# Kernel tuning notes

Measured on AMD Instinct MI355X. Metric: run time of the kernel, lower is better.

## Reference

```python
import jax, jax.numpy as jnp
import numpy as np

N, D, H, DK, DEG = 8192, 512, 8, 64, 16
E = N * DEG
M = N


def setup_inputs() -> dict:
    key = jax.random.key(0)
    ks = jax.random.split(key, 12)
    x = jax.random.normal(ks[0], (N, D), dtype=jnp.float32)
    # every node has DEG neighbors -> sorted row index, random cols
    row_index = jnp.repeat(jnp.arange(N, dtype=jnp.int64), DEG)
    col_index = jax.random.randint(ks[1], (E,), 0, M, dtype=jnp.int64)
    to_col_index = jax.random.randint(ks[2], (M,), 0, N, dtype=jnp.int64)
    att_bias = 0.1 * jax.random.normal(ks[3], (H, E), dtype=jnp.float32)
    pos = 10.0 * jax.random.uniform(ks[4], (N, 3), dtype=jnp.float32)
    col_pos = 10.0 * jax.random.uniform(ks[5], (M, 3), dtype=jnp.float32)
    dist = jnp.linalg.norm(col_pos[col_index] - pos[row_index], axis=-1)
    s = 1.0 / np.sqrt(D)
    Wq = s * jax.random.normal(ks[6], (H, DK, D), dtype=jnp.float32)
    Wqv = s * jax.random.normal(ks[7], (H, 3, D), dtype=jnp.float32)
    Wk = s * jax.random.normal(ks[8], (H, DK, D), dtype=jnp.float32)
    Wv = s * jax.random.normal(ks[9], (H, DK, D), dtype=jnp.float32)
    Wout = s * jax.random.normal(ks[10], (D, D + 4 * H), dtype=jnp.float32)
    bout = jnp.zeros((D,), dtype=jnp.float32)
    return {"x": x, "row_index": row_index, "col_index": col_index,
            "to_col_index": to_col_index, "att_bias": att_bias, "dist": dist,
            "pos": pos, "col_pos": col_pos, "Wq": Wq, "Wqv": Wqv, "Wk": Wk,
            "Wv": Wv, "Wout": Wout, "bout": bout}


def reference(x, row_index, col_index, to_col_index, att_bias, dist, pos,
              col_pos, Wq, Wqv, Wk, Wv, Wout, bout):
    n = x.shape[0]
    dk = Wq.shape[1]
    scale = 1.0 / jnp.sqrt(jnp.asarray(dk, x.dtype))
    # per-head projections: [H, N, dk]
    q = jnp.einsum('nd,hkd->hnk', x, Wq) * scale
    qv = jnp.einsum('nd,hkd->hnk', x, Wqv)              # [H, N, 3]
    kx = jnp.einsum('nd,hkd->hnk', x, Wk)[:, to_col_index]  # [H, M, dk]
    vx = jnp.einsum('nd,hkd->hnk', x, Wv)[:, to_col_index]
    # gather per edge -> [E, H, *]
    qe = q[:, row_index].transpose(1, 0, 2)
    ke = kx[:, col_index].transpose(1, 0, 2)
    qve = qv[:, row_index].transpose(1, 0, 2)           # [E, H, 3]
    rel = col_pos[col_index] - pos[row_index]           # [E, 3]
    dist_e = jnp.where(dist == 0, jnp.inf, dist)        # masked_fill(dist==0, inf)
    # angular = qv_row . col_pos_col - qv_row . pos_row = qv_row . rel
    angular = jnp.einsum('ehc,ec->eh', qve, rel)
    logit = jnp.einsum('ehk,ehk->eh', qe, ke) + att_bias.T + angular / dist_e[:, None]
    # sparse (per-row segment) softmax
    m = jax.ops.segment_max(logit, row_index, num_segments=n)
    p = jnp.exp(logit - m[row_index])
    s = jax.ops.segment_sum(p, row_index, num_segments=n)
    att = p / s[row_index]                              # [E, H]
    natt = att / dist_e[:, None]
    dst_vec = jax.ops.segment_sum(natt[:, :, None] * col_pos[col_index][:, None, :],
                                  row_index, num_segments=n)   # [N, H, 3]
    avg_inv_dist = jax.ops.segment_sum(natt, row_index, num_segments=n)  # [N, H]
    src_vec = avg_inv_dist[:, :, None] * pos[:, None, :]
    diff = dst_vec - src_vec
    feat3 = diff / jnp.maximum(jnp.linalg.norm(diff, axis=-1, keepdims=True), 1e-12)
    ve = vx[:, col_index].transpose(1, 0, 2)            # [E, H, dk]
    y = jax.ops.segment_sum(att[:, :, None] * ve, row_index, num_segments=n)  # [N, H, dk]
    feat = jnp.concatenate([y, feat3, avg_inv_dist[:, :, None]], axis=-1)
    feat = feat.reshape(n, -1)                          # [N, H*(dk+4)]
    return feat @ Wout.T + bout
```

## Files before the change

kernel.cpp:

```cpp
#include <hip/hip_runtime.h>
#include <math.h>

#define N_NODES 8192
#define D_FEAT  512
#define DEG     16
#define E_EDGES (N_NODES * DEG)
#define FEAT_W  576
#define FEAT_USED 544
#define OUT_W   512
#define QKV_W   1664

typedef unsigned short u16;
typedef __attribute__((ext_vector_type(8))) short short8;
typedef __attribute__((ext_vector_type(8))) unsigned short us8;
typedef __attribute__((ext_vector_type(4))) float f32x4;

__device__ __forceinline__ u16 f2bf(float f) {
    union { float f; unsigned u; } c; c.f = f;
    unsigned u = c.u;
    unsigned r = u + 0x7FFFu + ((u >> 16) & 1u);
    return (u16)(r >> 16);
}
__device__ __forceinline__ float bf2f(u16 h) {
    union { unsigned u; float f; } c; c.u = ((unsigned)h) << 16;
    return c.f;
}

__device__ __forceinline__ void async16(const void* g, void* l) {
    __builtin_amdgcn_global_load_lds(
        (const __attribute__((address_space(1))) void*)g,
        (__attribute__((address_space(3))) void*)l, 16, 0, 0);
}

__global__ __launch_bounds__(256) void gemm_qkv(
    const u16* __restrict__ xh, const u16* __restrict__ Bfuse,
    u16* __restrict__ qkv)
{
    __shared__ u16 smem[128 * 64 * 2];
    u16* sA = smem;
    u16* sB = smem + 128 * 64;

    const int tid = threadIdx.x;
    const int flat = blockIdx.x;
    const int xcd = flat & 7;
    const int rr  = flat >> 3;
    const int bm  = (xcd + 8 * (rr / 13)) * 128;
    const int bn  = (rr % 13) * 128;

    const int wave = tid >> 6;
    const int lane = tid & 63;
    const int wr   = (wave >> 1) * 64;
    const int wc   = (wave & 1) * 64;
    const int lrow = lane & 15;
    const int quad = lane >> 4;

    f32x4 acc[4][4];
    #pragma unroll
    for (int i = 0; i < 4; ++i)
        #pragma unroll
        for (int j = 0; j < 4; ++j) {
            f32x4 z = {0.f, 0.f, 0.f, 0.f};
            acc[i][j] = z;
        }

    for (int k0 = 0; k0 < 512; k0 += 64) {
        #pragma unroll
        for (int i = 0; i < 4; ++i) {
            const int lin = i * 256 + tid;
            const int row = lin >> 3;
            const int seg = ((lin & 7) ^ (row & 7)) << 3;
            async16(xh    + (size_t)(bm + row) * 512 + k0 + seg, sA + (lin << 3));
            async16(Bfuse + (size_t)(bn + row) * 512 + k0 + seg, sB + (lin << 3));
        }
        __syncthreads();

        #pragma unroll
        for (int ko = 0; ko < 64; ko += 32) {
            const int cbase = ko >> 3;
            short8 a_h[4], b_h[4];
            #pragma unroll
            for (int t = 0; t < 4; ++t) {
                const int ra = wr + t * 16 + lrow;
                const int rb = wc + t * 16 + lrow;
                a_h[t] = *(const short8*)&sA[ra * 64 + (((cbase + quad) ^ (ra & 7)) << 3)];
                b_h[t] = *(const short8*)&sB[rb * 64 + (((cbase + quad) ^ (rb & 7)) << 3)];
            }
            #pragma unroll
            for (int mt = 0; mt < 4; ++mt)
                #pragma unroll
                for (int nt = 0; nt < 4; ++nt)
                    acc[mt][nt] = __builtin_amdgcn_mfma_f32_16x16x32_bf16(
                        a_h[mt], b_h[nt], acc[mt][nt], 0, 0, 0);
        }
        __syncthreads();
    }

    u16* sC = smem;
    #pragma unroll
    for (int nt = 0; nt < 4; ++nt) {
        const int col = wc + nt * 16 + lrow;
        #pragma unroll
        for (int mt = 0; mt < 4; ++mt)
            #pragma unroll
            for (int r = 0; r < 4; ++r) {
                const int row = wr + mt * 16 + quad * 4 + r;
                sC[row * 128 + col] = f2bf(acc[mt][nt][r]);
            }
    }
    __syncthreads();
    #pragma unroll
    for (int p = 0; p < 8; ++p) {
        const int lin = p * 256 + tid;
        const int row = lin >> 4;
        const int c16 = lin & 15;
        *(uint4*)(qkv + (size_t)(bm + row) * QKV_W + bn + c16 * 8) =
            *(const uint4*)&sC[row * 128 + c16 * 8];
    }
}

__global__ __launch_bounds__(256) void gemm_out(
    const u16* __restrict__ feat, const u16* __restrict__ Woth,
    const float* __restrict__ bout, float* __restrict__ out)
{
    __shared__ u16 smem[64 * 64 + 128 * 64];
    u16* sA = smem;
    u16* sB = smem + 64 * 64;

    const int tid = threadIdx.x;
    const int flat = blockIdx.x;
    const int xcd = flat & 7;
    const int rr  = flat >> 3;
    const int bm  = (xcd + 8 * (rr / 4)) * 64;
    const int bn  = (rr % 4) * 128;

    const int wave = tid >> 6;
    const int lane = tid & 63;
    const int wr   = (wave >> 1) * 32;
    const int wc   = (wave & 1) * 64;
    const int lrow = lane & 15;
    const int quad = lane >> 4;

    f32x4 acc[2][4];
    #pragma unroll
    for (int i = 0; i < 2; ++i)
        #pragma unroll
        for (int j = 0; j < 4; ++j) {
            f32x4 z = {0.f, 0.f, 0.f, 0.f};
            acc[i][j] = z;
        }

    for (int k0 = 0; k0 < FEAT_W; k0 += 64) {
        #pragma unroll
        for (int i = 0; i < 2; ++i) {
            const int lin = i * 256 + tid;
            const int row = lin >> 3;
            const int seg = ((lin & 7) ^ (row & 7)) << 3;
            async16(feat + (size_t)(bm + row) * FEAT_W + k0 + seg, sA + (lin << 3));
        }
        #pragma unroll
        for (int i = 0; i < 4; ++i) {
            const int lin = i * 256 + tid;
            const int row = lin >> 3;
            const int seg = ((lin & 7) ^ (row & 7)) << 3;
            async16(Woth + (size_t)(bn + row) * FEAT_W + k0 + seg, sB + (lin << 3));
        }
        __syncthreads();

        #pragma unroll
        for (int ko = 0; ko < 64; ko += 32) {
            const int cbase = ko >> 3;
            short8 a_h[2], b_h[4];
            #pragma unroll
            for (int t = 0; t < 2; ++t) {
                const int ra = wr + t * 16 + lrow;
                a_h[t] = *(const short8*)&sA[ra * 64 + (((cbase + quad) ^ (ra & 7)) << 3)];
            }
            #pragma unroll
            for (int t = 0; t < 4; ++t) {
                const int rb = wc + t * 16 + lrow;
                b_h[t] = *(const short8*)&sB[rb * 64 + (((cbase + quad) ^ (rb & 7)) << 3)];
            }
            #pragma unroll
            for (int mt = 0; mt < 2; ++mt)
                #pragma unroll
                for (int nt = 0; nt < 4; ++nt)
                    acc[mt][nt] = __builtin_amdgcn_mfma_f32_16x16x32_bf16(
                        a_h[mt], b_h[nt], acc[mt][nt], 0, 0, 0);
        }
        __syncthreads();
    }

    #pragma unroll
    for (int nt = 0; nt < 4; ++nt) {
        const int col = bn + wc + nt * 16 + lrow;
        const float bb = bout[col];
        #pragma unroll
        for (int mt = 0; mt < 2; ++mt)
            #pragma unroll
            for (int r = 0; r < 4; ++r) {
                const int row = bm + wr + mt * 16 + quad * 4 + r;
                out[(size_t)row * OUT_W + col] = acc[mt][nt][r] + bb;
            }
    }
}

__global__ __launch_bounds__(256) void prep_kernel(
    const float* __restrict__ x,
    const float* __restrict__ Wq, const float* __restrict__ Wk,
    const float* __restrict__ Wv, const float* __restrict__ Wqv,
    const float* __restrict__ Wout,
    u16* __restrict__ xh, u16* __restrict__ B, u16* __restrict__ Woth)
{
    const int b = blockIdx.x;
    const int tid = threadIdx.x;
    if (b < 4096) {
        const int i = b * 256 + tid;
        const float4 v = ((const float4*)x)[i];
        ushort4 h;
        h.x = f2bf(v.x); h.y = f2bf(v.y); h.z = f2bf(v.z); h.w = f2bf(v.w);
        ((ushort4*)xh)[i] = h;
    } else if (b < 4928) {
        const int idx = (b - 4096) * 256 + tid;
        const int row = idx >> 7;
        const int c4  = idx & 127;
        float4 v = make_float4(0.f, 0.f, 0.f, 0.f);
        float scale = 1.f;
        if (row < 512) {
            v = *(const float4*)(Wq + (size_t)row * 512 + c4 * 4);
            scale = 0.125f;
        } else if (row < 1024) {
            v = *(const float4*)(Wk + (size_t)(row - 512) * 512 + c4 * 4);
        } else if (row < 1536) {
            v = *(const float4*)(Wv + (size_t)(row - 1024) * 512 + c4 * 4);
        } else if (row < 1560) {
            v = *(const float4*)(Wqv + (size_t)(row - 1536) * 512 + c4 * 4);
        }
        ushort4 h;
        h.x = f2bf(v.x * scale); h.y = f2bf(v.y * scale);
        h.z = f2bf(v.z * scale); h.w = f2bf(v.w * scale);
        ((ushort4*)B)[idx] = h;
    } else {
        const int i = (b - 4928) * 256 + tid;
        const int row = i / (FEAT_W / 4);
        const int c4  = i % (FEAT_W / 4);
        float4 v = make_float4(0.f, 0.f, 0.f, 0.f);
        if (c4 < FEAT_USED / 4)
            v = *(const float4*)(Wout + (size_t)row * FEAT_USED + c4 * 4);
        ushort4 h;
        h.x = f2bf(v.x); h.y = f2bf(v.y); h.z = f2bf(v.z); h.w = f2bf(v.w);
        ((ushort4*)Woth)[i] = h;
    }
}

__global__ __launch_bounds__(256) void edge_kernel(
    const u16* __restrict__ qkv,
    const int* __restrict__ col_index, const int* __restrict__ to_col,
    const float* __restrict__ att_bias, const float* __restrict__ dist,
    const float* __restrict__ pos, const float* __restrict__ col_pos,
    u16* __restrict__ feat)
{
    __shared__ float sLog[2][2][8][8];
    __shared__ float sY[2][512];
    __shared__ float sV[2][8][4];

    const int wave4 = threadIdx.x >> 6;
    const int nb = wave4 >> 1;
    const int w  = wave4 & 1;
    const int lane = threadIdx.x & 63;
    const int n = blockIdx.x * 2 + nb;
    const int h = lane >> 3;
    const int sub = lane & 7;
    const int hoff = lane * 8;

    const size_t qbase = (size_t)n * QKV_W;

    float qf[8];
    {
        const us8 qu = *(const us8*)(qkv + qbase + hoff);
        #pragma unroll
        for (int i = 0; i < 8; ++i) qf[i] = bf2f(qu[i]);
    }
    float qv0, qv1, qv2;
    {
        const float qvl = bf2f(qkv[qbase + 1536 + (lane < 24 ? lane : 0)]);
        qv0 = __shfl(qvl, h * 3 + 0);
        qv1 = __shfl(qvl, h * 3 + 1);
        qv2 = __shfl(qvl, h * 3 + 2);
    }
    const float px = pos[3 * n + 0], py = pos[3 * n + 1], pz = pos[3 * n + 2];

    const int j8 = lane & 7;
    const int e0 = n * DEG + w * 8 + j8;
    const int c_l  = col_index[e0];
    const int cc_l = to_col[c_l];
    const float d_l = dist[e0];
    const float invd_l = (d_l == 0.f) ? 0.f : (1.f / d_l);
    const float rx_l = col_pos[3 * c_l + 0] - px;
    const float ry_l = col_pos[3 * c_l + 1] - py;
    const float rz_l = col_pos[3 * c_l + 2] - pz;

    const float b_own = att_bias[(size_t)h * E_EDGES + n * DEG + w * 8 + sub];

    float logit[8];
    #pragma unroll
    for (int j = 0; j < 8; ++j) {
        const int cc = __shfl(cc_l, j);
        const us8 ku = *(const us8*)(qkv + (size_t)cc * QKV_W + 512 + hoff);
        float dot = 0.f;
        #pragma unroll
        for (int i = 0; i < 8; ++i) dot += qf[i] * bf2f(ku[i]);
        dot += __shfl_xor(dot, 1, 8);
        dot += __shfl_xor(dot, 2, 8);
        dot += __shfl_xor(dot, 4, 8);
        const float invd = __shfl(invd_l, j);
        const float ang = qv0 * __shfl(rx_l, j) + qv1 * __shfl(ry_l, j)
                        + qv2 * __shfl(rz_l, j);
        const float bj = __shfl(b_own, j, 8);
        logit[j] = dot + bj + ang * invd;
    }

    if (sub == 0) {
        #pragma unroll
        for (int j = 0; j < 8; ++j) sLog[nb][w][h][j] = logit[j];
    }
    __syncthreads();
    float lo[8];
    #pragma unroll
    for (int j = 0; j < 8; ++j) lo[j] = sLog[nb][1 - w][h][j];

    float m = logit[0];
    #pragma unroll
    for (int j = 1; j < 8; ++j) m = fmaxf(m, logit[j]);
    #pragma unroll
    for (int j = 0; j < 8; ++j) m = fmaxf(m, lo[j]);
    float s = 0.f;
    #pragma unroll
    for (int j = 0; j < 8; ++j) { logit[j] = __expf(logit[j] - m); s += logit[j]; }
    #pragma unroll
    for (int j = 0; j < 8; ++j) s += __expf(lo[j] - m);
    const float inv_s = 1.f / s;

    float y[8] = {0.f, 0.f, 0.f, 0.f, 0.f, 0.f, 0.f, 0.f};
    float dx = 0.f, dy = 0.f, dz = 0.f, aid = 0.f;
    #pragma unroll
    for (int j = 0; j < 8; ++j) {
        const float a = logit[j] * inv_s;
        const int cc = __shfl(cc_l, j);
        const us8 vu = *(const us8*)(qkv + (size_t)cc * QKV_W + 1024 + hoff);
        #pragma unroll
        for (int i = 0; i < 8; ++i) y[i] += a * bf2f(vu[i]);
        const float na = a * __shfl(invd_l, j);
        dx += na * __shfl(rx_l, j);
        dy += na * __shfl(ry_l, j);
        dz += na * __shfl(rz_l, j);
        aid += na;
    }

    if (w == 0) {
        #pragma unroll
        for (int i = 0; i < 8; ++i) sY[nb][hoff + i] = y[i];
        if (sub == 0) {
            sV[nb][h][0] = dx; sV[nb][h][1] = dy;
            sV[nb][h][2] = dz; sV[nb][h][3] = aid;
        }
    }
    __syncthreads();
    if (w == 1) {
        #pragma unroll
        for (int i = 0; i < 8; ++i) y[i] += sY[nb][hoff + i];

        u16* f = feat + (size_t)n * FEAT_W + h * 68;
        ushort4 o0, o1;
        o0.x = f2bf(y[0]); o0.y = f2bf(y[1]); o0.z = f2bf(y[2]); o0.w = f2bf(y[3]);
        o1.x = f2bf(y[4]); o1.y = f2bf(y[5]); o1.z = f2bf(y[6]); o1.w = f2bf(y[7]);
        *(ushort4*)(f + sub * 8 + 0) = o0;
        *(ushort4*)(f + sub * 8 + 4) = o1;
        if (sub == 0) {
            dx += sV[nb][h][0]; dy += sV[nb][h][1];
            dz += sV[nb][h][2]; aid += sV[nb][h][3];
            const float nrm = sqrtf(dx * dx + dy * dy + dz * dz);
            const float rn = 1.f / fmaxf(nrm, 1e-12f);
            ushort4 ex;
            ex.x = f2bf(dx * rn); ex.y = f2bf(dy * rn);
            ex.z = f2bf(dz * rn); ex.w = f2bf(aid);
            *(ushort4*)(f + 64) = ex;
        }
    }
}

extern "C" void kernel_launch(void* const* d_in, const int* in_sizes, int n_in,
                              void* d_out, int out_size, void* d_ws, size_t ws_size,
                              hipStream_t stream)
{
    const float* x         = (const float*)d_in[0];
    const int*   col_index = (const int*)d_in[2];
    const int*   to_col    = (const int*)d_in[3];
    const float* att_bias  = (const float*)d_in[4];
    const float* dist      = (const float*)d_in[5];
    const float* pos       = (const float*)d_in[6];
    const float* col_pos   = (const float*)d_in[7];
    const float* Wq        = (const float*)d_in[8];
    const float* Wqv       = (const float*)d_in[9];
    const float* Wk        = (const float*)d_in[10];
    const float* Wv        = (const float*)d_in[11];
    const float* Wout      = (const float*)d_in[12];
    const float* bout      = (const float*)d_in[13];
    float* out = (float*)d_out;

    char* ws = (char*)d_ws;
    u16* qkv   = (u16*)(ws + 0);
    u16* xh    = (u16*)(ws + 27262976);
    u16* Bfuse = (u16*)(ws + 35651584);
    u16* Woth  = (u16*)(ws + 37355520);
    u16* feat  = (u16*)(ws + 37945344);

    dim3 blk(256);

    hipLaunchKernelGGL(prep_kernel, dim3(5216), blk, 0, stream,
                       x, Wq, Wk, Wv, Wqv, Wout, xh, Bfuse, Woth);

    hipLaunchKernelGGL(gemm_qkv, dim3(832), blk, 0, stream, xh, Bfuse, qkv);

    hipLaunchKernelGGL(edge_kernel, dim3(N_NODES / 2), blk, 0, stream,
                       qkv, col_index, to_col, att_bias, dist, pos, col_pos, feat);

    hipLaunchKernelGGL(gemm_out, dim3(512), blk, 0, stream,
                       feat, Woth, bout, out);
}
```

Baseline: 162.0 us.

## Double-buffer QKV GEMM shared-memory tiles with async prefetch of next K slice

Restructures the QKV projection GEMM main loop into a two-stage ping-pong pipeline with K-step 32. Each iteration issues the async global-to-LDS loads for the next slice before running MFMAs on the current one, so load latency overlaps compute. It uses explicit waitcnt, barriers and sched_barriers with a new XOR swizzle for the narrower tile. The cost is twice as many loop iterations and barriers, plus manual scheduling fences that limit compiler reordering.

```diff
diff --git a/kernel.cpp b/kernel.cpp
--- a/kernel.cpp
+++ b/kernel.cpp
@@ -36,9 +36,7 @@
     const u16* __restrict__ xh, const u16* __restrict__ Bfuse,
     u16* __restrict__ qkv)
 {
-    __shared__ u16 smem[128 * 64 * 2];
-    u16* sA = smem;
-    u16* sB = smem + 128 * 64;
+    __shared__ u16 smem[2][2 * 128 * 32];
 
     const int tid = threadIdx.x;
     const int flat = blockIdx.x;
@@ -63,39 +61,56 @@
             acc[i][j] = z;
         }
 
-    for (int k0 = 0; k0 < 512; k0 += 64) {
-        #pragma unroll
-        for (int i = 0; i < 4; ++i) {
-            const int lin = i * 256 + tid;
-            const int row = lin >> 3;
-            const int seg = ((lin & 7) ^ (row & 7)) << 3;
-            async16(xh    + (size_t)(bm + row) * 512 + k0 + seg, sA + (lin << 3));
-            async16(Bfuse + (size_t)(bn + row) * 512 + k0 + seg, sB + (lin << 3));
-        }
-        __syncthreads();
-
-        #pragma unroll
-        for (int ko = 0; ko < 64; ko += 32) {
-            const int cbase = ko >> 3;
-            short8 a_h[4], b_h[4];
-            #pragma unroll
-            for (int t = 0; t < 4; ++t) {
-                const int ra = wr + t * 16 + lrow;
-                const int rb = wc + t * 16 + lrow;
-                a_h[t] = *(const short8*)&sA[ra * 64 + (((cbase + quad) ^ (ra & 7)) << 3)];
-                b_h[t] = *(const short8*)&sB[rb * 64 + (((cbase + quad) ^ (rb & 7)) << 3)];
-            }
-            #pragma unroll
-            for (int mt = 0; mt < 4; ++mt)
-                #pragma unroll
-                for (int nt = 0; nt < 4; ++nt)
-                    acc[mt][nt] = __builtin_amdgcn_mfma_f32_16x16x32_bf16(
-                        a_h[mt], b_h[nt], acc[mt][nt], 0, 0, 0);
-        }
-        __syncthreads();
-    }
-
-    u16* sC = smem;
+#define STAGE(bsel, k0) do {                                                 \
+        u16* _sA = &smem[bsel][0];                                           \
+        u16* _sB = &smem[bsel][128 * 32];                                    \
+        _Pragma("unroll")                                                    \
+        for (int i = 0; i < 2; ++i) {                                        \
+            const int lin = i * 256 + tid;                       \
+            const int row = lin >> 2;                                        \
+            const int seg = (((lin & 3) ^ ((row >> 1) & 3)) << 3);           \
+            async16(xh    + (size_t)(bm + row) * 512 + (k0) + seg, _sA + (lin << 3)); \
+            async16(Bfuse + (size_t)(bn + row) * 512 + (k0) + seg, _sB + (lin << 3)); \
+        }                                                                    \
+    } while (0)
+
+    STAGE(0, 0);
+    asm volatile("s_waitcnt vmcnt(0)" ::: "memory");
+    __builtin_amdgcn_s_barrier();
+    __builtin_amdgcn_sched_barrier(0);
+
+    #pragma unroll
+    for (int t = 0; t < 16; ++t) {
+        const int cur = t & 1;
+        if (t < 15) STAGE(cur ^ 1, (t + 1) * 32);
+
+        const u16* sA = &smem[cur][0];
+        const u16* sB = &smem[cur][128 * 32];
+        short8 a_h[4], b_h[4];
+        #pragma unroll
+        for (int tt = 0; tt < 4; ++tt) {
+            const int ra = wr + tt * 16 + lrow;
+            const int rb = wc + tt * 16 + lrow;
+            a_h[tt] = *(const short8*)&sA[ra * 32 + ((quad ^ ((ra >> 1) & 3)) << 3)];
+            b_h[tt] = *(const short8*)&sB[rb * 32 + ((quad ^ ((rb >> 1) & 3)) << 3)];
+        }
+        asm volatile("s_waitcnt lgkmcnt(0)" ::: "memory");
+        __builtin_amdgcn_sched_barrier(0);
+
+        #pragma unroll
+        for (int mt = 0; mt < 4; ++mt)
+            #pragma unroll
+            for (int nt = 0; nt < 4; ++nt)
+                acc[mt][nt] = __builtin_amdgcn_mfma_f32_16x16x32_bf16(
+                    a_h[mt], b_h[nt], acc[mt][nt], 0, 0, 0);
+
+        if (t < 15) asm volatile("s_waitcnt vmcnt(0)" ::: "memory");
+        __builtin_amdgcn_s_barrier();
+        __builtin_amdgcn_sched_barrier(0);
+    }
+#undef STAGE
+
+    u16* sC = &smem[0][0];
     #pragma unroll
     for (int nt = 0; nt < 4; ++nt) {
         const int col = wc + nt * 16 + lrow;
```

Measured after the change: 164.2 us. About the same (+1.4%).
